# Performance work log

Measured on AMD Instinct MI355X. Metric: run time of the kernel, lower is better.

Reference implementation:

```python
import jax, jax.numpy as jnp
import numpy as np

N_HEADS = 4
N_HIDDEN = 64  # out_features // n_heads
NEG_SLOPE = 0.2


def setup_inputs() -> dict:
    key = jax.random.key(0)
    k1, k2, k3, k4, k5 = jax.random.split(key, 5)
    B, N, F_IN, F_OUT = 1, 4096, 128, 256
    h = jax.random.normal(k1, (B, N, F_IN), dtype=jnp.float32)
    adj_mat = jax.random.uniform(k2, (N, N, 1), dtype=jnp.float32)
    W_proj = jax.random.normal(k3, (F_IN, N_HEADS * N_HIDDEN), dtype=jnp.float32) / np.sqrt(F_IN)
    W_proj_attn = jax.random.normal(k4, (F_IN, N_HEADS * N_HIDDEN // 2), dtype=jnp.float32) / np.sqrt(F_IN)
    w_attn = jax.random.normal(k5, (N_HIDDEN,), dtype=jnp.float32) / np.sqrt(N_HIDDEN)
    return {"h": h, "adj_mat": adj_mat, "W_proj": W_proj, "W_proj_attn": W_proj_attn, "w_attn": w_attn}


def reference(h, adj_mat, W_proj, W_proj_attn, w_attn):
    B, N, _ = h.shape
    H, D = N_HEADS, N_HIDDEN
    half = D // 2
    # value projection: (B, N, H, D)
    g = (h @ W_proj).reshape(B, N, H, D)
    # attention-feature projection: (B, N, H, D//2)
    ga = (h @ W_proj_attn).reshape(B, N, H, half)
    # attn(cat([ga_i, ga_j])) decomposes linearly: e_ij = <w_l, ga_i> + <w_r, ga_j>
    # (identical math to the torch repeat/cat/Linear, without the NxNxD tensor)
    el = jnp.einsum('bnhk,k->bnh', ga, w_attn[:half])   # dest node i term
    er = jnp.einsum('bnhk,k->bnh', ga, w_attn[half:])   # source node j term
    e = jax.nn.leaky_relu(el[:, :, None, :] + er[:, None, :, :], NEG_SLOPE)  # (B, N, N, H)
    mask = adj_mat >= 0.5  # (N, N, 1) broadcasts over (B, N, N, H)
    e = jnp.where(mask, e, -jnp.inf)
    a = jax.nn.softmax(e, axis=2)  # softmax over source nodes j
    # dropout is identity in eval mode
    out = jnp.einsum('bijh,bjhf->bihf', a, g)  # (B, N, H, D)
    return out.reshape(B, N, H * D)  # is_concat=True
```

## Files before the change

kernel.cpp:

```cpp
#include <hip/hip_runtime.h>
#include <hip/hip_bf16.h>

typedef __bf16 bf16_t;
typedef __bf16 bf16x4 __attribute__((ext_vector_type(4)));
typedef __bf16 bf16x8 __attribute__((ext_vector_type(8)));
typedef float floatx4 __attribute__((ext_vector_type(4)));

#define N_NODES 4096
#define F_IN 128
#define NUM_HEADS 4
#define D_HID 64
#define F_OUT 256
#define NEG_SLOPE 0.2f

__global__ __launch_bounds__(384) void proj_kernel(
    const float* __restrict__ hmat, const float* __restrict__ Wp,
    const float* __restrict__ Wa, const float* __restrict__ wattn,
    bf16_t* __restrict__ GB, float* __restrict__ el,
    float* __restrict__ E1r, float* __restrict__ E2r)
{
    __shared__ float hl[4][F_IN];
    const int t = threadIdx.x;
    const int j0 = blockIdx.x * 4;

    if (t < 128) {
        const int jl = t >> 5, m0 = (t & 31) * 4;
        *reinterpret_cast<float4*>(&hl[jl][m0]) =
            *reinterpret_cast<const float4*>(&hmat[(size_t)(j0 + jl) * F_IN + m0]);
    }
    __syncthreads();

    float acc[4] = {0.f, 0.f, 0.f, 0.f};

    const float* wptr;
    int stride;
    if (t < 256) { wptr = Wp + t;         stride = 256; }
    else         { wptr = Wa + (t - 256); stride = 128; }

    for (int m = 0; m < F_IN; m += 4) {
        const float w0 = wptr[(size_t)(m + 0) * stride];
        const float w1 = wptr[(size_t)(m + 1) * stride];
        const float w2 = wptr[(size_t)(m + 2) * stride];
        const float w3 = wptr[(size_t)(m + 3) * stride];
#pragma unroll
        for (int jl = 0; jl < 4; ++jl) {
            const float4 hv = *reinterpret_cast<const float4*>(&hl[jl][m]);
            acc[jl] = fmaf(hv.w, w3, fmaf(hv.z, w2, fmaf(hv.y, w1, fmaf(hv.x, w0, acc[jl]))));
        }
    }

    if (t < 256) {
        const int h = t >> 6, f = t & 63;
        bf16x4 o;
#pragma unroll
        for (int q = 0; q < 4; ++q) o[q] = (bf16_t)acc[q];
        const size_t base = ((((size_t)h * 128 + (j0 >> 5)) * 4 + (f >> 4)) * 64
                             + (f & 15) + 16 * ((j0 >> 3) & 3)) * 8 + (j0 & 7);
        *reinterpret_cast<bf16x4*>(&GB[base]) = o;
    } else {
        const int ta = t - 256;
        const int ha = ta >> 5, k = ta & 31;
        const float wl = wattn[k], wr = wattn[32 + k];
#pragma unroll
        for (int jl = 0; jl < 4; ++jl) {
            float vl = acc[jl] * wl;
            float vr = acc[jl] * wr;
#pragma unroll
            for (int s = 16; s >= 1; s >>= 1) {
                vl += __shfl_xor(vl, s, 64);
                vr += __shfl_xor(vr, s, 64);
            }
            if (k == 0) {
                el[ha * N_NODES + j0 + jl]  = vl;
                E1r[ha * N_NODES + j0 + jl] = __expf(vr);
                E2r[ha * N_NODES + j0 + jl] = __expf(NEG_SLOPE * vr);
            }
        }
    }
}

__global__ __launch_bounds__(256, 4) void attn_kernel(
    const float* __restrict__ adj, const bf16_t* __restrict__ GB,
    const float* __restrict__ el, const float* __restrict__ E1r,
    const float* __restrict__ E2r,
    float* __restrict__ numout, float* __restrict__ den_g,
    int njc, int ntiles)
{
    const int tid = threadIdx.x;
    const int i0  = blockIdx.x * 16;
    const int jc  = blockIdx.y;
    const int jT0 = jc * ntiles * 64;

    const int hh   = tid >> 6;
    const int lane = tid & 63;
    const int m    = lane & 15;
    const int quad = lane >> 4;

    const float eli = el[hh * N_NODES + i0 + m];
    const float E1i = __expf(eli);
    const float E2i = __expf(NEG_SLOPE * eli);
    const float Ti  = __expf(-eli);

    const float* adjl = adj + (size_t)(i0 + m) * N_NODES + quad * 8;
    const float* E1p  = E1r + hh * N_NODES + quad * 8;
    const float* E2p  = E2r + hh * N_NODES + quad * 8;
    const bf16_t* gb0 = GB + (size_t)hh * 128 * 2048 + lane * 8;

    floatx4 acc0 = {0.f, 0.f, 0.f, 0.f};
    floatx4 acc1 = acc0, acc2 = acc0, acc3 = acc0, accd = acc0;
    bf16x8 ones;
#pragma unroll
    for (int q = 0; q < 8; ++q) ones[q] = (bf16_t)1.0f;

#pragma unroll 2
    for (int k = 0; k < ntiles; ++k) {
        const int jT = jT0 + k * 64;
        const bf16_t* gbb = gb0 + (size_t)(jT >> 5) * 2048;

#pragma unroll
        for (int kt = 0; kt < 2; ++kt) {
            const int jk = jT + kt * 32;
            const float4 aa  = *reinterpret_cast<const float4*>(adjl + jk);
            const float4 ab  = *reinterpret_cast<const float4*>(adjl + jk + 4);
            const float4 e1a = *reinterpret_cast<const float4*>(E1p + jk);
            const float4 e1b = *reinterpret_cast<const float4*>(E1p + jk + 4);
            const float4 e2a = *reinterpret_cast<const float4*>(E2p + jk);
            const float4 e2b = *reinterpret_cast<const float4*>(E2p + jk + 4);

            bf16x8 af;
            af[0] = (aa.x >= 0.5f) ? (bf16_t)((e1a.x > Ti) ? E1i * e1a.x : E2i * e2a.x) : (bf16_t)0.f;
            af[1] = (aa.y >= 0.5f) ? (bf16_t)((e1a.y > Ti) ? E1i * e1a.y : E2i * e2a.y) : (bf16_t)0.f;
            af[2] = (aa.z >= 0.5f) ? (bf16_t)((e1a.z > Ti) ? E1i * e1a.z : E2i * e2a.z) : (bf16_t)0.f;
            af[3] = (aa.w >= 0.5f) ? (bf16_t)((e1a.w > Ti) ? E1i * e1a.w : E2i * e2a.w) : (bf16_t)0.f;
            af[4] = (ab.x >= 0.5f) ? (bf16_t)((e1b.x > Ti) ? E1i * e1b.x : E2i * e2b.x) : (bf16_t)0.f;
            af[5] = (ab.y >= 0.5f) ? (bf16_t)((e1b.y > Ti) ? E1i * e1b.y : E2i * e2b.y) : (bf16_t)0.f;
            af[6] = (ab.z >= 0.5f) ? (bf16_t)((e1b.z > Ti) ? E1i * e1b.z : E2i * e2b.z) : (bf16_t)0.f;
            af[7] = (ab.w >= 0.5f) ? (bf16_t)((e1b.w > Ti) ? E1i * e1b.w : E2i * e2b.w) : (bf16_t)0.f;

            const bf16x8 b0 = *reinterpret_cast<const bf16x8*>(gbb + kt * 2048);
            const bf16x8 b1 = *reinterpret_cast<const bf16x8*>(gbb + kt * 2048 + 512);
            const bf16x8 b2 = *reinterpret_cast<const bf16x8*>(gbb + kt * 2048 + 1024);
            const bf16x8 b3 = *reinterpret_cast<const bf16x8*>(gbb + kt * 2048 + 1536);

            accd = __builtin_amdgcn_mfma_f32_16x16x32_bf16(af, ones, accd, 0, 0, 0);
            acc0 = __builtin_amdgcn_mfma_f32_16x16x32_bf16(af, b0, acc0, 0, 0, 0);
            acc1 = __builtin_amdgcn_mfma_f32_16x16x32_bf16(af, b1, acc1, 0, 0, 0);
            acc2 = __builtin_amdgcn_mfma_f32_16x16x32_bf16(af, b2, acc2, 0, 0, 0);
            acc3 = __builtin_amdgcn_mfma_f32_16x16x32_bf16(af, b3, acc3, 0, 0, 0);
        }
    }

    const int ibase = i0 + quad * 4;
    if (njc == 1) {
#pragma unroll
        for (int rr = 0; rr < 4; ++rr) {
            const float rd = 1.0f / accd[rr];
            float* dst = numout + (size_t)(ibase + rr) * F_OUT + hh * D_HID + m;
            dst[0]  = acc0[rr] * rd;
            dst[16] = acc1[rr] * rd;
            dst[32] = acc2[rr] * rd;
            dst[48] = acc3[rr] * rd;
        }
    } else {
        float* nrow = numout + (size_t)jc * ((size_t)N_NODES * F_OUT);
#pragma unroll
        for (int rr = 0; rr < 4; ++rr) {
            float* dst = nrow + (size_t)(ibase + rr) * F_OUT + hh * D_HID + m;
            dst[0]  = acc0[rr];
            dst[16] = acc1[rr];
            dst[32] = acc2[rr];
            dst[48] = acc3[rr];
        }
        if (m == 0) {
#pragma unroll
            for (int rr = 0; rr < 4; ++rr)
                den_g[((size_t)jc * N_NODES + ibase + rr) * NUM_HEADS + hh] = accd[rr];
        }
    }
}

__global__ __launch_bounds__(256) void reduce_kernel(
    const float* __restrict__ num, const float* __restrict__ den,
    float* __restrict__ out, int njc)
{
    const int idx = blockIdx.x * 256 + threadIdx.x;
    const int i  = idx >> 8;
    const int c  = idx & 255;
    const int hh = c >> 6;
    float n = 0.f, d = 0.f;
    for (int jc = 0; jc < njc; ++jc) {
        n += num[(size_t)jc * ((size_t)N_NODES * F_OUT) + idx];
        d += den[((size_t)jc * N_NODES + i) * NUM_HEADS + hh];
    }
    out[idx] = n / d;
}

extern "C" void kernel_launch(void* const* d_in, const int* in_sizes, int n_in,
                              void* d_out, int out_size, void* d_ws, size_t ws_size,
                              hipStream_t stream)
{
    const float* hmat = (const float*)d_in[0];
    const float* adj  = (const float*)d_in[1];
    const float* Wp   = (const float*)d_in[2];
    const float* Wa   = (const float*)d_in[3];
    const float* watt = (const float*)d_in[4];
    float* out = (float*)d_out;

    char* ws = (char*)d_ws;
    bf16_t* GB  = (bf16_t*)ws;
    float*  el  = (float*)(ws + (2ull << 20));
    float*  E1r = (float*)(ws + (2ull << 20) + (64ull << 10));
    float*  E2r = (float*)(ws + (2ull << 20) + (128ull << 10));
    const size_t baseoff = (2ull << 20) + (192ull << 10);

    const size_t num_bytes = (size_t)N_NODES * F_OUT * 4;
    const size_t den_bytes = (size_t)N_NODES * NUM_HEADS * 4;
    const int njc = (ws_size >= baseoff + 4 * (num_bytes + den_bytes)) ? 4 : 2;

    float* num = (float*)(ws + baseoff);
    float* den = (float*)(ws + baseoff + (size_t)njc * num_bytes);

    proj_kernel<<<1024, 384, 0, stream>>>(hmat, Wp, Wa, watt, GB, el, E1r, E2r);
    attn_kernel<<<dim3(256, njc), 256, 0, stream>>>(adj, GB, el, E1r, E2r,
                                                    num, den, njc, (N_NODES / njc) / 64);
    reduce_kernel<<<(N_NODES * F_OUT) / 256, 256, 0, stream>>>(num, den, out, njc);
}
```

Baseline: 179.3 us.

## Pack adjacency into bitmask and compute two row tiles per wave with split-K reduction

```diff
diff --git a/kernel.cpp b/kernel.cpp
--- a/kernel.cpp
+++ b/kernel.cpp
@@ -5,6 +5,7 @@
 typedef __bf16 bf16x4 __attribute__((ext_vector_type(4)));
 typedef __bf16 bf16x8 __attribute__((ext_vector_type(8)));
 typedef float floatx4 __attribute__((ext_vector_type(4)));
+typedef unsigned long long u64;
 
 #define N_NODES 4096
 #define F_IN 128
@@ -12,6 +13,21 @@
 #define D_HID 64
 #define F_OUT 256
 #define NEG_SLOPE 0.2f
+
+__global__ __launch_bounds__(256) void mask_kernel(
+    const float* __restrict__ adj, u64* __restrict__ mask)
+{
+    const int w    = blockIdx.x * 4 + (threadIdx.x >> 6);
+    const int lane = threadIdx.x & 63;
+    const float* row = adj + (size_t)w * N_NODES + lane;
+    u64* mrow = mask + (size_t)w * 64;
+#pragma unroll 4
+    for (int c = 0; c < 64; ++c) {
+        const float v = row[c * 64];
+        const u64 b = __ballot(v >= 0.5f);
+        if (lane == 0) mrow[c] = b;
+    }
+}
 
 __global__ __launch_bounds__(384) void proj_kernel(
     const float* __restrict__ hmat, const float* __restrict__ Wp,
@@ -79,119 +95,144 @@
     }
 }
 
-__global__ __launch_bounds__(256, 4) void attn_kernel(
-    const float* __restrict__ adj, const bf16_t* __restrict__ GB,
+__global__ __launch_bounds__(1024, 4) void attn_kernel(
+    const u64* __restrict__ mask, const bf16_t* __restrict__ GB,
     const float* __restrict__ el, const float* __restrict__ E1r,
     const float* __restrict__ E2r,
-    float* __restrict__ numout, float* __restrict__ den_g,
-    int njc, int ntiles)
-{
-    const int tid = threadIdx.x;
-    const int i0  = blockIdx.x * 16;
-    const int jc  = blockIdx.y;
-    const int jT0 = jc * ntiles * 64;
-
-    const int hh   = tid >> 6;
+    float* __restrict__ num, float* __restrict__ den_g)
+{
+    __shared__ float lbuf[NUM_HEADS * 2 * 20 * 64];
+
+    const int tid  = threadIdx.x;
+    const int i0   = blockIdx.x * 32;
+    const int jc   = blockIdx.y;
+    const int wave = tid >> 6;
+    const int hh   = wave & 3;
+    const int js   = wave >> 2;
     const int lane = tid & 63;
     const int m    = lane & 15;
     const int quad = lane >> 4;
 
-    const float eli = el[hh * N_NODES + i0 + m];
-    const float E1i = __expf(eli);
-    const float E2i = __expf(NEG_SLOPE * eli);
-    const float Ti  = __expf(-eli);
-
-    const float* adjl = adj + (size_t)(i0 + m) * N_NODES + quad * 8;
-    const float* E1p  = E1r + hh * N_NODES + quad * 8;
-    const float* E2p  = E2r + hh * N_NODES + quad * 8;
+    const int row0 = i0 + m, row1 = row0 + 16;
+    const float el0 = el[hh * N_NODES + row0];
+    const float el1 = el[hh * N_NODES + row1];
+    const float E1i0 = __expf(el0), E2i0 = __expf(NEG_SLOPE * el0), Ti0 = __expf(-el0);
+    const float E1i1 = __expf(el1), E2i1 = __expf(NEG_SLOPE * el1), Ti1 = __expf(-el1);
+
+    const u64* mrow0 = mask + (size_t)row0 * 64;
+    const u64* mrow1 = mask + (size_t)row1 * 64;
+    const float* E1p = E1r + hh * N_NODES + quad * 8;
+    const float* E2p = E2r + hh * N_NODES + quad * 8;
     const bf16_t* gb0 = GB + (size_t)hh * 128 * 2048 + lane * 8;
 
-    floatx4 acc0 = {0.f, 0.f, 0.f, 0.f};
-    floatx4 acc1 = acc0, acc2 = acc0, acc3 = acc0, accd = acc0;
+    floatx4 a00 = {0.f, 0.f, 0.f, 0.f};
+    floatx4 a01 = a00, a02 = a00, a03 = a00, ad0 = a00;
+    floatx4 a10 = a00, a11 = a00, a12 = a00, a13 = a00, ad1 = a00;
     bf16x8 ones;
 #pragma unroll
     for (int q = 0; q < 8; ++q) ones[q] = (bf16_t)1.0f;
 
 #pragma unroll 2
-    for (int k = 0; k < ntiles; ++k) {
-        const int jT = jT0 + k * 64;
-        const bf16_t* gbb = gb0 + (size_t)(jT >> 5) * 2048;
+    for (int t = 0; t < 8; ++t) {
+        const int kk = jc * 32 + js + t * 4;
+        const u64 M0 = mrow0[kk];
+        const u64 M1 = mrow1[kk];
+        const bf16_t* gbb = gb0 + (size_t)kk * 4096;
+        const int jb = kk * 64;
 
 #pragma unroll
         for (int kt = 0; kt < 2; ++kt) {
-            const int jk = jT + kt * 32;
-            const float4 aa  = *reinterpret_cast<const float4*>(adjl + jk);
-            const float4 ab  = *reinterpret_cast<const float4*>(adjl + jk + 4);
+            const int jk = jb + kt * 32;
             const float4 e1a = *reinterpret_cast<const float4*>(E1p + jk);
             const float4 e1b = *reinterpret_cast<const float4*>(E1p + jk + 4);
             const float4 e2a = *reinterpret_cast<const float4*>(E2p + jk);
             const float4 e2b = *reinterpret_cast<const float4*>(E2p + jk + 4);
 
-            bf16x8 af;
-            af[0] = (aa.x >= 0.5f) ? (bf16_t)((e1a.x > Ti) ? E1i * e1a.x : E2i * e2a.x) : (bf16_t)0.f;
-            af[1] = (aa.y >= 0.5f) ? (bf16_t)((e1a.y > Ti) ? E1i * e1a.y : E2i * e2a.y) : (bf16_t)0.f;
-            af[2] = (aa.z >= 0.5f) ? (bf16_t)((e1a.z > Ti) ? E1i * e1a.z : E2i * e2a.z) : (bf16_t)0.f;
-            af[3] = (aa.w >= 0.5f) ? (bf16_t)((e1a.w > Ti) ? E1i * e1a.w : E2i * e2a.w) : (bf16_t)0.f;
-            af[4] = (ab.x >= 0.5f) ? (bf16_t)((e1b.x > Ti) ? E1i * e1b.x : E2i * e2b.x) : (bf16_t)0.f;
-            af[5] = (ab.y >= 0.5f) ? (bf16_t)((e1b.y > Ti) ? E1i * e1b.y : E2i * e2b.y) : (bf16_t)0.f;
-            af[6] = (ab.z >= 0.5f) ? (bf16_t)((e1b.z > Ti) ? E1i * e1b.z : E2i * e2b.z) : (bf16_t)0.f;
-            af[7] = (ab.w >= 0.5f) ? (bf16_t)((e1b.w > Ti) ? E1i * e1b.w : E2i * e2b.w) : (bf16_t)0.f;
-
-            const bf16x8 b0 = *reinterpret_cast<const bf16x8*>(gbb + kt * 2048);
-            const bf16x8 b1 = *reinterpret_cast<const bf16x8*>(gbb + kt * 2048 + 512);
-            const bf16x8 b2 = *reinterpret_cast<const bf16x8*>(gbb + kt * 2048 + 1024);
-            const bf16x8 b3 = *reinterpret_cast<const bf16x8*>(gbb + kt * 2048 + 1536);
-
-            accd = __builtin_amdgcn_mfma_f32_16x16x32_bf16(af, ones, accd, 0, 0, 0);
-            acc0 = __builtin_amdgcn_mfma_f32_16x16x32_bf16(af, b0, acc0, 0, 0, 0);
-            acc1 = __builtin_amdgcn_mfma_f32_16x16x32_bf16(af, b1, acc1, 0, 0, 0);
-            acc2 = __builtin_amdgcn_mfma_f32_16x16x32_bf16(af, b2, acc2, 0, 0, 0);
-            acc3 = __builtin_amdgcn_mfma_f32_16x16x32_bf16(af, b3, acc3, 0, 0, 0);
-        }
-    }
-
-    const int ibase = i0 + quad * 4;
-    if (njc == 1) {
+            const unsigned int b0 = ((unsigned int)(M0 >> (kt * 32)) >> (quad * 8)) & 0xffu;
+            const unsigned int b1 = ((unsigned int)(M1 >> (kt * 32)) >> (quad * 8)) & 0xffu;
+
+            const bf16x8 g0 = *reinterpret_cast<const bf16x8*>(gbb + kt * 2048);
+            const bf16x8 g1 = *reinterpret_cast<const bf16x8*>(gbb + kt * 2048 + 512);
+            const bf16x8 g2 = *reinterpret_cast<const bf16x8*>(gbb + kt * 2048 + 1024);
+            const bf16x8 g3 = *reinterpret_cast<const bf16x8*>(gbb + kt * 2048 + 1536);
+
+            const float pe1[8] = {e1a.x, e1a.y, e1a.z, e1a.w, e1b.x, e1b.y, e1b.z, e1b.w};
+            const float pe2[8] = {e2a.x, e2a.y, e2a.z, e2a.w, e2b.x, e2b.y, e2b.z, e2b.w};
+
+            bf16x8 af0, af1;
+#pragma unroll
+            for (int q = 0; q < 8; ++q) {
+                const float p0 = (pe1[q] > Ti0) ? E1i0 * pe1[q] : E2i0 * pe2[q];
+                const float p1 = (pe1[q] > Ti1) ? E1i1 * pe1[q] : E2i1 * pe2[q];
+                af0[q] = ((b0 >> q) & 1u) ? (bf16_t)p0 : (bf16_t)0.f;
+                af1[q] = ((b1 >> q) & 1u) ? (bf16_t)p1 : (bf16_t)0.f;
+            }
+
+            ad0 = __builtin_amdgcn_mfma_f32_16x16x32_bf16(af0, ones, ad0, 0, 0, 0);
+            a00 = __builtin_amdgcn_mfma_f32_16x16x32_bf16(af0, g0, a00, 0, 0, 0);
+            a01 = __builtin_amdgcn_mfma_f32_16x16x32_bf16(af0, g1, a01, 0, 0, 0);
+            a02 = __builtin_amdgcn_mfma_f32_16x16x32_bf16(af0, g2, a02, 0, 0, 0);
+            a03 = __builtin_amdgcn_mfma_f32_16x16x32_bf16(af0, g3, a03, 0, 0, 0);
+            ad1 = __builtin_amdgcn_mfma_f32_16x16x32_bf16(af1, ones, ad1, 0, 0, 0);
+            a10 = __builtin_amdgcn_mfma_f32_16x16x32_bf16(af1, g0, a10, 0, 0, 0);
+            a11 = __builtin_amdgcn_mfma_f32_16x16x32_bf16(af1, g1, a11, 0, 0, 0);
+            a12 = __builtin_amdgcn_mfma_f32_16x16x32_bf16(af1, g2, a12, 0, 0, 0);
+            a13 = __builtin_amdgcn_mfma_f32_16x16x32_bf16(af1, g3, a13, 0, 0, 0);
+        }
+    }
+
+    floatx4* mine[10] = {&a00, &a01, &a02, &a03, &ad0, &a10, &a11, &a12, &a13, &ad1};
+    for (int s = 1; s < 4; ++s) {
+        if (js == s) {
+#pragma unroll
+            for (int c = 0; c < 10; ++c) {
+                const floatx4 v = *mine[c];
+#pragma unroll
+                for (int r = 0; r < 4; ++r)
+                    lbuf[((hh * 10 + c) * 4 + r) * 64 + lane] = v[r];
+            }
+        }
+        __syncthreads();
+        if (js == 0) {
+#pragma unroll
+            for (int c = 0; c < 10; ++c) {
+#pragma unroll
+                for (int r = 0; r < 4; ++r)
+                    (*mine[c])[r] += lbuf[((hh * 10 + c) * 4 + r) * 64 + lane];
+            }
+        }
+        __syncthreads();
+    }
+
+    if (js == 0) {
+        float* nrow = num + (size_t)jc * ((size_t)N_NODES * F_OUT);
 #pragma unroll
         for (int rr = 0; rr < 4; ++rr) {
-            const float rd = 1.0f / accd[rr];
-            float* dst = numout + (size_t)(ibase + rr) * F_OUT + hh * D_HID + m;
-            dst[0]  = acc0[rr] * rd;
-            dst[16] = acc1[rr] * rd;
-            dst[32] = acc2[rr] * rd;
-            dst[48] = acc3[rr] * rd;
-        }
-    } else {
-        float* nrow = numout + (size_t)jc * ((size_t)N_NODES * F_OUT);
-#pragma unroll
-        for (int rr = 0; rr < 4; ++rr) {
-            float* dst = nrow + (size_t)(ibase + rr) * F_OUT + hh * D_HID + m;
-            dst[0]  = acc0[rr];
-            dst[16] = acc1[rr];
-            dst[32] = acc2[rr];
-            dst[48] = acc3[rr];
-        }
-        if (m == 0) {
-#pragma unroll
-            for (int rr = 0; rr < 4; ++rr)
-                den_g[((size_t)jc * N_NODES + ibase + rr) * NUM_HEADS + hh] = accd[rr];
+            const int ib0 = i0 + quad * 4 + rr;
+            const int ib1 = ib0 + 16;
+            float* d0 = nrow + (size_t)ib0 * F_OUT + hh * D_HID + m;
+            float* d1 = nrow + (size_t)ib1 * F_OUT + hh * D_HID + m;
+            d0[0] = a00[rr]; d0[16] = a01[rr]; d0[32] = a02[rr]; d0[48] = a03[rr];
+            d1[0] = a10[rr]; d1[16] = a11[rr]; d1[32] = a12[rr]; d1[48] = a13[rr];
+            if (m == 0) {
+                den_g[((size_t)jc * N_NODES + ib0) * NUM_HEADS + hh] = ad0[rr];
+                den_g[((size_t)jc * N_NODES + ib1) * NUM_HEADS + hh] = ad1[rr];
+            }
         }
     }
 }
 
 __global__ __launch_bounds__(256) void reduce_kernel(
     const float* __restrict__ num, const float* __restrict__ den,
-    float* __restrict__ out, int njc)
+    float* __restrict__ out)
 {
     const int idx = blockIdx.x * 256 + threadIdx.x;
     const int i  = idx >> 8;
     const int c  = idx & 255;
     const int hh = c >> 6;
-    float n = 0.f, d = 0.f;
-    for (int jc = 0; jc < njc; ++jc) {
-        n += num[(size_t)jc * ((size_t)N_NODES * F_OUT) + idx];
-        d += den[((size_t)jc * N_NODES + i) * NUM_HEADS + hh];
-    }
+    const float n = num[idx] + num[(size_t)N_NODES * F_OUT + idx];
+    const float d = den[(size_t)i * NUM_HEADS + hh]
+                  + den[((size_t)N_NODES + i) * NUM_HEADS + hh];
     out[idx] = n / d;
 }
 
@@ -211,17 +252,14 @@
     float*  el  = (float*)(ws + (2ull << 20));
     float*  E1r = (float*)(ws + (2ull << 20) + (64ull << 10));
     float*  E2r = (float*)(ws + (2ull << 20) + (128ull << 10));
-    const size_t baseoff = (2ull << 20) + (192ull << 10);
-
-    const size_t num_bytes = (size_t)N_NODES * F_OUT * 4;
-    const size_t den_bytes = (size_t)N_NODES * NUM_HEADS * 4;
-    const int njc = (ws_size >= baseoff + 4 * (num_bytes + den_bytes)) ? 4 : 2;
+    u64*    msk = (u64*)  (ws + (2ull << 20) + (192ull << 10));
+    const size_t baseoff = (4ull << 20) + (192ull << 10);
 
     float* num = (float*)(ws + baseoff);
-    float* den = (float*)(ws + baseoff + (size_t)njc * num_bytes);
-
+    float* den = (float*)(ws + baseoff + 2ull * N_NODES * F_OUT * 4);
+
+    mask_kernel<<<1024, 256, 0, stream>>>(adj, msk);
     proj_kernel<<<1024, 384, 0, stream>>>(hmat, Wp, Wa, watt, GB, el, E1r, E2r);
-    attn_kernel<<<dim3(256, njc), 256, 0, stream>>>(adj, GB, el, E1r, E2r,
-                                                    num, den, njc, (N_NODES / njc) / 64);
-    reduce_kernel<<<(N_NODES * F_OUT) / 256, 256, 0, stream>>>(num, den, out, njc);
-}
+    attn_kernel<<<dim3(128, 2), 1024, 0, stream>>>(msk, GB, el, E1r, E2r, num, den);
+    reduce_kernel<<<(N_NODES * F_OUT) / 256, 256, 0, stream>>>(num, den, out);
+}
```

New measurement: 179.6 us. Within noise of the previous version (+0.2%).
